# Kernel optimization log

Hardware: AMD Instinct MI355X
Metric: run time of the kernel (lower is better)

Reference implementation:

```python
import jax, jax.numpy as jnp
import numpy as np


def setup_inputs() -> dict:
    key = jax.random.key(0)
    k1, k2, k3, k4 = jax.random.split(key, 4)
    B, Sq, Sk, d = 16, 2048, 2048, 64
    queries = jax.random.normal(k1, (B, Sq, d), dtype=jnp.float32)
    keys = jax.random.normal(k2, (B, Sk, d), dtype=jnp.float32)
    values = jax.random.normal(k3, (B, Sk, d), dtype=jnp.float32)
    # True = padded key position (masked out)
    key_padding_mask = jax.random.randint(k4, (B, Sk), 0, 2) == 1
    return {"queries": queries, "keys": keys, "values": values,
            "key_padding_mask": key_padding_mask}


def reference(queries, keys, values, key_padding_mask):
    d = queries.shape[-1]
    # scores: [B, Sq, Sk]
    scores = jnp.einsum("bqd,bkd->bqk", queries, keys) / jnp.sqrt(
        jnp.asarray(d, dtype=queries.dtype))
    # padded keys get -inf before softmax (mask broadcast over query dim)
    scores = jnp.where(key_padding_mask[:, None, :], -jnp.inf, scores)
    attention_weights = jax.nn.softmax(scores, axis=2)
    return jnp.einsum("bqk,bkd->bqd", attention_weights, values)
```

## Files before the change

kernel.cpp:

```cpp
#include <hip/hip_runtime.h>
#include <hip/hip_bf16.h>

#define NB 16
#define SQ 2048
#define SK 2048
#define DH 64

#define KBLK 1024
#define VBLK 512
#define BBLK 128

typedef __attribute__((ext_vector_type(8))) short short8;
typedef __attribute__((ext_vector_type(8))) __bf16 bf16x8;
typedef __attribute__((ext_vector_type(4))) float floatx4;
typedef __attribute__((ext_vector_type(16))) float floatx16;
typedef __attribute__((ext_vector_type(2))) unsigned uint2v;

#define GLOB const __attribute__((address_space(1))) void*
#define LDSP __attribute__((address_space(3))) void*

__device__ __forceinline__ unsigned pk2(float a, float b) {
  __hip_bfloat162 h = __float22bfloat162_rn(make_float2(a, b));
  unsigned u; __builtin_memcpy(&u, &h, 4); return u;
}
__device__ __forceinline__ floatx16 mfma32(short8 a, short8 b, floatx16 c) {
  return __builtin_amdgcn_mfma_f32_32x32x16_bf16(
      __builtin_bit_cast(bf16x8, a), __builtin_bit_cast(bf16x8, b), c, 0, 0, 0);
}

__device__ __forceinline__ int swap23(int k) {
  return (((k >> 2) ^ (k >> 3)) & 1) ? (k ^ 12) : k;
}

__global__ __launch_bounds__(256)
void prepass(const float* __restrict__ K, const float* __restrict__ V,
             const int* __restrict__ m, short* __restrict__ Kb,
             short* __restrict__ Vt, float* __restrict__ bias) {
  __shared__ unsigned tlw[64 * 33];
  const int blk = blockIdx.x;
  const int t = threadIdx.x;
  if (blk < KBLK) {
    size_t i8 = ((size_t)blk * 256 + t) * 8;
    floatx4 a = *(const floatx4*)(K + i8);
    floatx4 b = *(const floatx4*)(K + i8 + 4);
    union { unsigned u[4]; short8 s; } w;
    w.u[0] = pk2(a[0], a[1]); w.u[1] = pk2(a[2], a[3]);
    w.u[2] = pk2(b[0], b[1]); w.u[3] = pk2(b[2], b[3]);
    const int local = (int)(i8 & 4095);
    const int key = local >> 6, chunk = (local >> 3) & 7;
    const int prow = swap23(key);
    const size_t tb = i8 & ~(size_t)4095;
    *(short8*)(Kb + tb + prow * 64 + ((chunk ^ (prow & 7)) << 3)) = w.s;
  } else if (blk < KBLK + VBLK) {
    const int bt = blk - KBLK;
    const int key2 = t & 31;
    const int dg = (t >> 5) * 8;
    const float* vp0 = V + ((size_t)bt * 64 + 2 * key2) * 64 + dg;
    const float* vp1 = vp0 + 64;
    floatx4 va  = *(const floatx4*)(vp0);
    floatx4 va2 = *(const floatx4*)(vp0 + 4);
    floatx4 vb  = *(const floatx4*)(vp1);
    floatx4 vb2 = *(const floatx4*)(vp1 + 4);
#pragma unroll
    for (int j = 0; j < 4; ++j) {
      tlw[(dg + j) * 33 + key2]     = pk2(va[j],  vb[j]);
      tlw[(dg + 4 + j) * 33 + key2] = pk2(va2[j], vb2[j]);
    }
    __syncthreads();
    const short* tls = (const short*)tlw;
    short* dst = Vt + (size_t)bt * 4096;
#pragma unroll
    for (int i = 0; i < 2; ++i) {
      int idx = i * 2048 + t * 8;
      int d = idx >> 6, key = idx & 63;
      int chunk = key >> 3;
      *(short8*)(dst + d * 64 + ((chunk ^ (d & 7)) << 3)) =
          *(const short8*)(tls + d * 66 + key);
    }
  } else {
    int i = (blk - KBLK - VBLK) * 256 + t;
    bias[i] = m[i] ? -1e30f : 0.0f;
  }
}

__global__ __launch_bounds__(256, 4)
void attn_main(const float* __restrict__ Q, const short* __restrict__ Kb,
               const short* __restrict__ Vt, const float* __restrict__ bias,
               float* __restrict__ Out, float* __restrict__ Op,
               float* __restrict__ lsum) {
  __shared__ __align__(16) short ks[2][4096];
  __shared__ __align__(16) short vt[2][4096];
  __shared__ __align__(16) float bsh[512];

  const int gid = blockIdx.x;
  const int xcd = gid & 7;
  const int j   = gid >> 3;
  const int cmb = xcd + 8 * (j >> 4);
  const int part = cmb >> 4;
  const int b    = cmb & 15;
  const int qt   = j & 15;
  const int tid  = threadIdx.x;
  const int wave = tid >> 6;
  const int lane = tid & 63;
  const int n32  = lane & 31;
  const int h    = lane >> 5;
  const int sw   = n32 & 7;
  const int q0   = qt * 128 + wave * 32;
  const int kt0  = part << 3;

  const float QS = 0.125f * 1.4426950408889634f;
  short8 qf[4];
  {
    const float* qp = Q + ((size_t)b * SQ + q0 + n32) * DH + 8 * h;
#pragma unroll
    for (int c = 0; c < 4; ++c) {
      floatx4 a  = *(const floatx4*)(qp + 16 * c);
      floatx4 a2 = *(const floatx4*)(qp + 16 * c + 4);
      union { unsigned u[4]; short8 s; } w;
      w.u[0] = pk2(a[0] * QS, a[1] * QS);
      w.u[1] = pk2(a[2] * QS, a[3] * QS);
      w.u[2] = pk2(a2[0] * QS, a2[1] * QS);
      w.u[3] = pk2(a2[2] * QS, a2[3] * QS);
      qf[c] = w.s;
    }
  }

  if (tid < 128) {
    floatx4 bv = *(const floatx4*)(bias + (size_t)b * SK + kt0 * 64 + tid * 4);
    *(floatx4*)(bsh + tid * 4) = bv;
  }

  floatx16 o0, o1;
#pragma unroll
  for (int i = 0; i < 16; ++i) { o0[i] = 0.f; o1[i] = 0.f; }
  float l_q = 0.f;

  const short* kg = Kb + ((size_t)b * SK + (size_t)kt0 * 64) * DH;
  const short* vg = Vt + ((size_t)b * 32 + kt0) * 4096;

  const int lo0 = (wave * 2) * 512;
  const int lo1 = (wave * 2 + 1) * 512;
  const int go0 = lo0 + lane * 8;
  const int go1 = lo1 + lane * 8;

#define ISSUE_K(tile, buf) do {                                                        \
    const short* kn_ = kg + (size_t)(tile) * 4096;                                     \
    __builtin_amdgcn_global_load_lds((GLOB)(kn_ + go0), (LDSP)&ks[buf][lo0], 16, 0, 0);\
    __builtin_amdgcn_global_load_lds((GLOB)(kn_ + go1), (LDSP)&ks[buf][lo1], 16, 0, 0);\
  } while (0)
#define ISSUE_V(tile, buf) do {                                                        \
    const short* vn_ = vg + (size_t)(tile) * 4096;                                     \
    __builtin_amdgcn_global_load_lds((GLOB)(vn_ + go0), (LDSP)&vt[buf][lo0], 16, 0, 0);\
    __builtin_amdgcn_global_load_lds((GLOB)(vn_ + go1), (LDSP)&vt[buf][lo1], 16, 0, 0);\
  } while (0)

  floatx16 sA[2], sB[2];

#define QK(tt, d) do {                                                                 \
    const float* bq_ = bsh + (tt) * 64 + 8 * h;                                        \
    _Pragma("unroll") for (int u = 0; u < 4; ++u) {                                    \
      const int off_ = 16 * (u >> 1) + 4 * (u & 1);                                    \
      floatx4 bv0_ = *(const floatx4*)(bq_ + off_);                                    \
      floatx4 bv1_ = *(const floatx4*)(bq_ + 32 + off_);                               \
      _Pragma("unroll") for (int i = 0; i < 4; ++i) {                                  \
        sA[d][4 * u + i] = bv0_[i]; sB[d][4 * u + i] = bv1_[i]; } }                    \
    _Pragma("unroll") for (int c = 0; c < 4; ++c) {                                    \
      short8 kf0_ = *(short8*)(ks[(tt) & 1] + n32 * 64        + ((2 * c + h) ^ sw) * 8);\
      short8 kf1_ = *(short8*)(ks[(tt) & 1] + (32 + n32) * 64 + ((2 * c + h) ^ sw) * 8);\
      sA[d] = mfma32(kf0_, qf[c], sA[d]);                                              \
      sB[d] = mfma32(kf1_, qf[c], sB[d]); }                                            \
  } while (0)

  asm volatile("s_waitcnt vmcnt(0) lgkmcnt(0)" ::: "memory");
  __builtin_amdgcn_sched_barrier(0);
  ISSUE_K(0, 0); ISSUE_V(0, 0); ISSUE_K(1, 1); ISSUE_V(1, 1);
  asm volatile("s_waitcnt vmcnt(6)" ::: "memory");
  __builtin_amdgcn_s_barrier();
  __builtin_amdgcn_sched_barrier(0);
  QK(0, 0);

#pragma unroll
  for (int t = 0; t < 8; ++t) {
    if (t < 7) asm volatile("s_waitcnt vmcnt(2)" ::: "memory");
    else       asm volatile("s_waitcnt vmcnt(0)" ::: "memory");
    __builtin_amdgcn_s_barrier();
    __builtin_amdgcn_sched_barrier(0);

    if (t < 6) ISSUE_K(t + 2, t & 1);

    uint2v pka[4], pkb[4];
    {
      float rs = 0.f;
#pragma unroll
      for (int u = 0; u < 4; ++u) {
        float p0 = __builtin_amdgcn_exp2f(sA[t & 1][4 * u + 0]);
        float p1 = __builtin_amdgcn_exp2f(sA[t & 1][4 * u + 1]);
        float p2 = __builtin_amdgcn_exp2f(sA[t & 1][4 * u + 2]);
        float p3 = __builtin_amdgcn_exp2f(sA[t & 1][4 * u + 3]);
        float r0 = __builtin_amdgcn_exp2f(sB[t & 1][4 * u + 0]);
        float r1 = __builtin_amdgcn_exp2f(sB[t & 1][4 * u + 1]);
        float r2 = __builtin_amdgcn_exp2f(sB[t & 1][4 * u + 2]);
        float r3 = __builtin_amdgcn_exp2f(sB[t & 1][4 * u + 3]);
        rs += ((p0 + p1) + (p2 + p3)) + ((r0 + r1) + (r2 + r3));
        pka[u].x = pk2(p0, p1); pka[u].y = pk2(p2, p3);
        pkb[u].x = pk2(r0, r1); pkb[u].y = pk2(r2, r3);
      }
      l_q += rs;
    }
    if (t < 7) QK(t + 1, (t + 1) & 1);

#pragma unroll
    for (int c = 0; c < 4; ++c) {
      const uint2v* X = (c < 2) ? pka : pkb;
      union { unsigned u[4]; short8 s; } pf;
      pf.u[0] = X[2 * (c & 1)].x;     pf.u[1] = X[2 * (c & 1)].y;
      pf.u[2] = X[2 * (c & 1) + 1].x; pf.u[3] = X[2 * (c & 1) + 1].y;
      short8 vf0 = *(short8*)(vt[t & 1] + n32 * 64        + ((2 * c + h) ^ sw) * 8);
      short8 vf1 = *(short8*)(vt[t & 1] + (32 + n32) * 64 + ((2 * c + h) ^ sw) * 8);
      o0 = mfma32(vf0, pf.s, o0);
      o1 = mfma32(vf1, pf.s, o1);
    }

    if (t < 6) {
      __builtin_amdgcn_s_barrier();
      __builtin_amdgcn_sched_barrier(0);
      ISSUE_V(t + 2, t & 1);
    }
  }
#undef ISSUE_K
#undef ISSUE_V
#undef QK

  l_q += __shfl_xor(l_q, 32);

  float* Od = part ? (Op + (size_t)(part - 1) * NB * SQ * DH) : Out;
  float* orow = Od + ((size_t)b * SQ + q0 + n32) * DH;
#pragma unroll
  for (int u = 0; u < 4; ++u) {
    floatx4 w0, w1;
#pragma unroll
    for (int i = 0; i < 4; ++i) { w0[i] = o0[4 * u + i]; w1[i] = o1[4 * u + i]; }
    *(floatx4*)(orow + 8 * u + 4 * h)      = w0;
    *(floatx4*)(orow + 32 + 8 * u + 4 * h) = w1;
  }
  if (lane < 32)
    lsum[(size_t)part * NB * SQ + (size_t)b * SQ + q0 + lane] = l_q;
}

__global__ __launch_bounds__(256)
void combine(const float* __restrict__ Op, const float* __restrict__ lsum,
             float* __restrict__ Out) {
  int idx = blockIdx.x * 256 + threadIdx.x;
  int q = idx >> 3;
  int dc = (idx & 7) * 8;
  float inv = 1.0f / (lsum[q] + lsum[NB * SQ + q] +
                      lsum[2 * NB * SQ + q] + lsum[3 * NB * SQ + q]);
  const size_t base = (size_t)q * DH + dc;
  const size_t stride = (size_t)NB * SQ * DH;
  floatx4 a0 = *(const floatx4*)(Out + base);
  floatx4 a1 = *(const floatx4*)(Out + base + 4);
  floatx4 b0 = *(const floatx4*)(Op + base);
  floatx4 b1 = *(const floatx4*)(Op + base + 4);
  floatx4 c0 = *(const floatx4*)(Op + stride + base);
  floatx4 c1 = *(const floatx4*)(Op + stride + base + 4);
  floatx4 d0 = *(const floatx4*)(Op + 2 * stride + base);
  floatx4 d1 = *(const floatx4*)(Op + 2 * stride + base + 4);
  *(floatx4*)(Out + base)     = (a0 + b0 + c0 + d0) * inv;
  *(floatx4*)(Out + base + 4) = (a1 + b1 + c1 + d1) * inv;
}

extern "C" void kernel_launch(void* const* d_in, const int* in_sizes, int n_in,
                              void* d_out, int out_size, void* d_ws, size_t ws_size,
                              hipStream_t stream) {
  const float* Q = (const float*)d_in[0];
  const float* K = (const float*)d_in[1];
  const float* V = (const float*)d_in[2];
  const int* mask = (const int*)d_in[3];
  float* Out = (float*)d_out;

  char* ws = (char*)d_ws;
  short* Kb   = (short*)(ws);
  short* Vt   = (short*)(ws + 4194304);
  float* bias = (float*)(ws + 8388608);
  float* lsum = (float*)(ws + 8519680);
  float* Op   = (float*)(ws + 9043968);

  prepass  <<<KBLK + VBLK + BBLK, 256, 0, stream>>>(K, V, mask, Kb, Vt, bias);
  attn_main<<<4 * NB * (SQ / 128), 256, 0, stream>>>(Q, Kb, Vt, bias, Out, Op, lsum);
  combine  <<<NB * SQ * DH / 8 / 256, 256, 0, stream>>>(Op, lsum, Out);
}
```

Before: 110.9 us.

## Drop split-K partitioning; each block processes all key tiles and normalizes in-kernel

Removes the 4-way split over the key dimension and the separate combine kernel. Each block now loops over all 32 key tiles, loads the full bias row into shared memory, and divides by the row sum before writing output. This removes the partial-output writes, the lsum buffer and the extra launch and its memory traffic. The cost is a 4x smaller grid (256 blocks), which may underfill the GPU's compute units, plus a launch_bounds occupancy hint of 1.

```diff
diff --git a/kernel.cpp b/kernel.cpp
--- a/kernel.cpp
+++ b/kernel.cpp
@@ -83,22 +83,19 @@
   }
 }
 
-__global__ __launch_bounds__(256, 4)
+__global__ __launch_bounds__(256, 1)
 void attn_main(const float* __restrict__ Q, const short* __restrict__ Kb,
                const short* __restrict__ Vt, const float* __restrict__ bias,
-               float* __restrict__ Out, float* __restrict__ Op,
-               float* __restrict__ lsum) {
+               float* __restrict__ Out) {
   __shared__ __align__(16) short ks[2][4096];
   __shared__ __align__(16) short vt[2][4096];
-  __shared__ __align__(16) float bsh[512];
+  __shared__ __align__(16) float bsh[2048];
 
   const int gid = blockIdx.x;
   const int xcd = gid & 7;
   const int j   = gid >> 3;
-  const int cmb = xcd + 8 * (j >> 4);
-  const int part = cmb >> 4;
-  const int b    = cmb & 15;
-  const int qt   = j & 15;
+  const int b   = xcd + 8 * (j >> 4);
+  const int qt  = j & 15;
   const int tid  = threadIdx.x;
   const int wave = tid >> 6;
   const int lane = tid & 63;
@@ -106,7 +103,6 @@
   const int h    = lane >> 5;
   const int sw   = n32 & 7;
   const int q0   = qt * 128 + wave * 32;
-  const int kt0  = part << 3;
 
   const float QS = 0.125f * 1.4426950408889634f;
   short8 qf[4];
@@ -125,9 +121,10 @@
     }
   }
 
-  if (tid < 128) {
-    floatx4 bv = *(const floatx4*)(bias + (size_t)b * SK + kt0 * 64 + tid * 4);
-    *(floatx4*)(bsh + tid * 4) = bv;
+  {
+    const float* bp = bias + (size_t)b * SK + tid * 8;
+    *(floatx4*)(bsh + tid * 8)     = *(const floatx4*)(bp);
+    *(floatx4*)(bsh + tid * 8 + 4) = *(const floatx4*)(bp + 4);
   }
 
   floatx16 o0, o1;
@@ -135,8 +132,8 @@
   for (int i = 0; i < 16; ++i) { o0[i] = 0.f; o1[i] = 0.f; }
   float l_q = 0.f;
 
-  const short* kg = Kb + ((size_t)b * SK + (size_t)kt0 * 64) * DH;
-  const short* vg = Vt + ((size_t)b * 32 + kt0) * 4096;
+  const short* kg = Kb + (size_t)b * SK * DH;
+  const short* vg = Vt + (size_t)b * 32 * 4096;
 
   const int lo0 = (wave * 2) * 512;
   const int lo1 = (wave * 2 + 1) * 512;
@@ -179,14 +176,14 @@
   __builtin_amdgcn_sched_barrier(0);
   QK(0, 0);
 
-#pragma unroll
-  for (int t = 0; t < 8; ++t) {
-    if (t < 7) asm volatile("s_waitcnt vmcnt(2)" ::: "memory");
-    else       asm volatile("s_waitcnt vmcnt(0)" ::: "memory");
+#pragma unroll 2
+  for (int t = 0; t < 32; ++t) {
+    if (t < 31) asm volatile("s_waitcnt vmcnt(2)" ::: "memory");
+    else        asm volatile("s_waitcnt vmcnt(0)" ::: "memory");
     __builtin_amdgcn_s_barrier();
     __builtin_amdgcn_sched_barrier(0);
 
-    if (t < 6) ISSUE_K(t + 2, t & 1);
+    if (t < 30) ISSUE_K(t + 2, t & 1);
 
     uint2v pka[4], pkb[4];
     {
@@ -207,7 +204,7 @@
       }
       l_q += rs;
     }
-    if (t < 7) QK(t + 1, (t + 1) & 1);
+    if (t < 31) QK(t + 1, (t + 1) & 1);
 
 #pragma unroll
     for (int c = 0; c < 4; ++c) {
@@ -221,7 +218,7 @@
       o1 = mfma32(vf1, pf.s, o1);
     }
 
-    if (t < 6) {
+    if (t < 30) {
       __builtin_amdgcn_s_barrier();
       __builtin_amdgcn_sched_barrier(0);
       ISSUE_V(t + 2, t & 1);
@@ -232,41 +229,17 @@
 #undef QK
 
   l_q += __shfl_xor(l_q, 32);
-
-  float* Od = part ? (Op + (size_t)(part - 1) * NB * SQ * DH) : Out;
-  float* orow = Od + ((size_t)b * SQ + q0 + n32) * DH;
+  const float inv = 1.0f / l_q;
+
+  float* orow = Out + ((size_t)b * SQ + q0 + n32) * DH;
 #pragma unroll
   for (int u = 0; u < 4; ++u) {
     floatx4 w0, w1;
 #pragma unroll
-    for (int i = 0; i < 4; ++i) { w0[i] = o0[4 * u + i]; w1[i] = o1[4 * u + i]; }
+    for (int i = 0; i < 4; ++i) { w0[i] = o0[4 * u + i] * inv; w1[i] = o1[4 * u + i] * inv; }
     *(floatx4*)(orow + 8 * u + 4 * h)      = w0;
     *(floatx4*)(orow + 32 + 8 * u + 4 * h) = w1;
   }
-  if (lane < 32)
-    lsum[(size_t)part * NB * SQ + (size_t)b * SQ + q0 + lane] = l_q;
-}
-
-__global__ __launch_bounds__(256)
-void combine(const float* __restrict__ Op, const float* __restrict__ lsum,
-             float* __restrict__ Out) {
-  int idx = blockIdx.x * 256 + threadIdx.x;
-  int q = idx >> 3;
-  int dc = (idx & 7) * 8;
-  float inv = 1.0f / (lsum[q] + lsum[NB * SQ + q] +
-                      lsum[2 * NB * SQ + q] + lsum[3 * NB * SQ + q]);
-  const size_t base = (size_t)q * DH + dc;
-  const size_t stride = (size_t)NB * SQ * DH;
-  floatx4 a0 = *(const floatx4*)(Out + base);
-  floatx4 a1 = *(const floatx4*)(Out + base + 4);
-  floatx4 b0 = *(const floatx4*)(Op + base);
-  floatx4 b1 = *(const floatx4*)(Op + base + 4);
-  floatx4 c0 = *(const floatx4*)(Op + stride + base);
-  floatx4 c1 = *(const floatx4*)(Op + stride + base + 4);
-  floatx4 d0 = *(const floatx4*)(Op + 2 * stride + base);
-  floatx4 d1 = *(const floatx4*)(Op + 2 * stride + base + 4);
-  *(floatx4*)(Out + base)     = (a0 + b0 + c0 + d0) * inv;
-  *(floatx4*)(Out + base + 4) = (a1 + b1 + c1 + d1) * inv;
 }
 
 extern "C" void kernel_launch(void* const* d_in, const int* in_sizes, int n_in,
@@ -282,10 +255,7 @@
   short* Kb   = (short*)(ws);
   short* Vt   = (short*)(ws + 4194304);
   float* bias = (float*)(ws + 8388608);
-  float* lsum = (float*)(ws + 8519680);
-  float* Op   = (float*)(ws + 9043968);
 
   prepass  <<<KBLK + VBLK + BBLK, 256, 0, stream>>>(K, V, mask, Kb, Vt, bias);
-  attn_main<<<4 * NB * (SQ / 128), 256, 0, stream>>>(Q, Kb, Vt, bias, Out, Op, lsum);
-  combine  <<<NB * SQ * DH / 8 / 256, 256, 0, stream>>>(Op, lsum, Out);
-}
+  attn_main<<<NB * (SQ / 128), 256, 0, stream>>>(Q, Kb, Vt, bias, Out);
+}
```

After: 111.3 us. Within noise of the previous version (+0.3%).

## Halve key-split partitions to two and add MFMA priority hints

Applied to the files above, without the earlier changes.

Reduces the split-K attention from four key partitions to two, so each block processes 16 key tiles instead of 8 and the grid shrinks to 512 blocks. The combine kernel now reads and sums only two partial outputs, which cuts partial-output traffic and reloading of Q. The block-to-data mapping is changed so all key partitions of a batch land on the same XCD, the launch-bounds occupancy hint is lowered, the main loop is only partially unrolled, and s_setprio is raised around the MFMA sections. The risk is fewer blocks and therefore less parallelism to hide latency.

```diff
diff --git a/kernel.cpp b/kernel.cpp
--- a/kernel.cpp
+++ b/kernel.cpp
@@ -9,6 +9,9 @@
 #define KBLK 1024
 #define VBLK 512
 #define BBLK 128
+
+#define NPART 2
+#define NT 16
 
 typedef __attribute__((ext_vector_type(8))) short short8;
 typedef __attribute__((ext_vector_type(8))) __bf16 bf16x8;
@@ -83,22 +86,22 @@
   }
 }
 
-__global__ __launch_bounds__(256, 4)
+__global__ __launch_bounds__(256, 2)
 void attn_main(const float* __restrict__ Q, const short* __restrict__ Kb,
                const short* __restrict__ Vt, const float* __restrict__ bias,
                float* __restrict__ Out, float* __restrict__ Op,
                float* __restrict__ lsum) {
   __shared__ __align__(16) short ks[2][4096];
   __shared__ __align__(16) short vt[2][4096];
-  __shared__ __align__(16) float bsh[512];
+  __shared__ __align__(16) float bsh[1024];
 
   const int gid = blockIdx.x;
   const int xcd = gid & 7;
   const int j   = gid >> 3;
-  const int cmb = xcd + 8 * (j >> 4);
-  const int part = cmb >> 4;
-  const int b    = cmb & 15;
-  const int qt   = j & 15;
+  const int b   = xcd + 8 * (j >> 5);
+  const int rem = j & 31;
+  const int part = rem >> 4;
+  const int qt   = rem & 15;
   const int tid  = threadIdx.x;
   const int wave = tid >> 6;
   const int lane = tid & 63;
@@ -106,7 +109,7 @@
   const int h    = lane >> 5;
   const int sw   = n32 & 7;
   const int q0   = qt * 128 + wave * 32;
-  const int kt0  = part << 3;
+  const int kt0  = part * NT;
 
   const float QS = 0.125f * 1.4426950408889634f;
   short8 qf[4];
@@ -125,7 +128,7 @@
     }
   }
 
-  if (tid < 128) {
+  {
     floatx4 bv = *(const floatx4*)(bias + (size_t)b * SK + kt0 * 64 + tid * 4);
     *(floatx4*)(bsh + tid * 4) = bv;
   }
@@ -164,11 +167,13 @@
       floatx4 bv1_ = *(const floatx4*)(bq_ + 32 + off_);                               \
       _Pragma("unroll") for (int i = 0; i < 4; ++i) {                                  \
         sA[d][4 * u + i] = bv0_[i]; sB[d][4 * u + i] = bv1_[i]; } }                    \
+    __builtin_amdgcn_s_setprio(1);                                                     \
     _Pragma("unroll") for (int c = 0; c < 4; ++c) {                                    \
       short8 kf0_ = *(short8*)(ks[(tt) & 1] + n32 * 64        + ((2 * c + h) ^ sw) * 8);\
       short8 kf1_ = *(short8*)(ks[(tt) & 1] + (32 + n32) * 64 + ((2 * c + h) ^ sw) * 8);\
       sA[d] = mfma32(kf0_, qf[c], sA[d]);                                              \
       sB[d] = mfma32(kf1_, qf[c], sB[d]); }                                            \
+    __builtin_amdgcn_s_setprio(0);                                                     \
   } while (0)
 
   asm volatile("s_waitcnt vmcnt(0) lgkmcnt(0)" ::: "memory");
@@ -179,14 +184,14 @@
   __builtin_amdgcn_sched_barrier(0);
   QK(0, 0);
 
-#pragma unroll
-  for (int t = 0; t < 8; ++t) {
-    if (t < 7) asm volatile("s_waitcnt vmcnt(2)" ::: "memory");
-    else       asm volatile("s_waitcnt vmcnt(0)" ::: "memory");
+#pragma unroll 2
+  for (int t = 0; t < NT; ++t) {
+    if (t < NT - 1) asm volatile("s_waitcnt vmcnt(2)" ::: "memory");
+    else            asm volatile("s_waitcnt vmcnt(0)" ::: "memory");
     __builtin_amdgcn_s_barrier();
     __builtin_amdgcn_sched_barrier(0);
 
-    if (t < 6) ISSUE_K(t + 2, t & 1);
+    if (t < NT - 2) ISSUE_K(t + 2, t & 1);
 
     uint2v pka[4], pkb[4];
     {
@@ -207,8 +212,9 @@
       }
       l_q += rs;
     }
-    if (t < 7) QK(t + 1, (t + 1) & 1);
-
+    if (t < NT - 1) QK(t + 1, (t + 1) & 1);
+
+    __builtin_amdgcn_s_setprio(1);
 #pragma unroll
     for (int c = 0; c < 4; ++c) {
       const uint2v* X = (c < 2) ? pka : pkb;
@@ -220,8 +226,9 @@
       o0 = mfma32(vf0, pf.s, o0);
       o1 = mfma32(vf1, pf.s, o1);
     }
-
-    if (t < 6) {
+    __builtin_amdgcn_s_setprio(0);
+
+    if (t < NT - 2) {
       __builtin_amdgcn_s_barrier();
       __builtin_amdgcn_sched_barrier(0);
       ISSUE_V(t + 2, t & 1);
@@ -233,7 +240,7 @@
 
   l_q += __shfl_xor(l_q, 32);
 
-  float* Od = part ? (Op + (size_t)(part - 1) * NB * SQ * DH) : Out;
+  float* Od = part ? Op : Out;
   float* orow = Od + ((size_t)b * SQ + q0 + n32) * DH;
 #pragma unroll
   for (int u = 0; u < 4; ++u) {
@@ -253,20 +260,14 @@
   int idx = blockIdx.x * 256 + threadIdx.x;
   int q = idx >> 3;
   int dc = (idx & 7) * 8;
-  float inv = 1.0f / (lsum[q] + lsum[NB * SQ + q] +
-                      lsum[2 * NB * SQ + q] + lsum[3 * NB * SQ + q]);
+  float inv = 1.0f / (lsum[q] + lsum[NB * SQ + q]);
   const size_t base = (size_t)q * DH + dc;
-  const size_t stride = (size_t)NB * SQ * DH;
   floatx4 a0 = *(const floatx4*)(Out + base);
   floatx4 a1 = *(const floatx4*)(Out + base + 4);
   floatx4 b0 = *(const floatx4*)(Op + base);
   floatx4 b1 = *(const floatx4*)(Op + base + 4);
-  floatx4 c0 = *(const floatx4*)(Op + stride + base);
-  floatx4 c1 = *(const floatx4*)(Op + stride + base + 4);
-  floatx4 d0 = *(const floatx4*)(Op + 2 * stride + base);
-  floatx4 d1 = *(const floatx4*)(Op + 2 * stride + base + 4);
-  *(floatx4*)(Out + base)     = (a0 + b0 + c0 + d0) * inv;
-  *(floatx4*)(Out + base + 4) = (a1 + b1 + c1 + d1) * inv;
+  *(floatx4*)(Out + base)     = (a0 + b0) * inv;
+  *(floatx4*)(Out + base + 4) = (a1 + b1) * inv;
 }
 
 extern "C" void kernel_launch(void* const* d_in, const int* in_sizes, int n_in,
@@ -283,9 +284,9 @@
   short* Vt   = (short*)(ws + 4194304);
   float* bias = (float*)(ws + 8388608);
   float* lsum = (float*)(ws + 8519680);
-  float* Op   = (float*)(ws + 9043968);
+  float* Op   = (float*)(ws + 8781824);
 
   prepass  <<<KBLK + VBLK + BBLK, 256, 0, stream>>>(K, V, mask, Kb, Vt, bias);
-  attn_main<<<4 * NB * (SQ / 128), 256, 0, stream>>>(Q, Kb, Vt, bias, Out, Op, lsum);
+  attn_main<<<NPART * NB * (SQ / 128), 256, 0, stream>>>(Q, Kb, Vt, bias, Out, Op, lsum);
   combine  <<<NB * SQ * DH / 8 / 256, 256, 0, stream>>>(Op, lsum, Out);
 }
```

Result: faster. 108.0 us (-2.6%).
